# Optimization experiments

Measured on AMD Instinct MI355X. Metric: run time of the kernel, lower is better.

Reference implementation:

```python
import jax, jax.numpy as jnp
import numpy as np
from jax import lax

H = 4096          # hidden_size
NH = 32           # num_attention_heads
NKV = 8           # num_key_value_heads
HD = H // NH      # head_dim = 128
CACHE = 2048      # state_length (kv cache length)
POS = 1024        # current decode position
THETA = 10000.0


def _rope_tables():
    inv_freq = 1.0 / (THETA ** (np.arange(0, HD, 2, dtype=np.float32) / HD))
    t = np.arange(CACHE * 2, dtype=np.float32)
    freqs = np.einsum('i,j->ij', t, inv_freq)          # [2*CACHE, HD/2]
    emb = np.concatenate([freqs, freqs], axis=-1)      # [2*CACHE, HD]
    return (jnp.asarray(np.cos(emb)[None]),            # [1, 2*CACHE, HD]
            jnp.asarray(np.sin(emb)[None]))


def setup_inputs() -> dict:
    key = jax.random.key(0)
    ks = jax.random.split(key, 8)
    cos_cached, sin_cached = _rope_tables()
    # additive causal mask for decode: positions <= current_pos visible
    mask = jnp.where(jnp.arange(CACHE) <= POS, 0.0, -1e9).astype(jnp.float32)
    return {
        'hidden_states': jax.random.normal(ks[0], (1, 1, H), dtype=jnp.float32),
        'attention_mask': mask.reshape(1, 1, 1, CACHE),
        'key_cache': jax.random.normal(ks[1], (1, NKV, CACHE, HD), dtype=jnp.float32),
        'value_cache': jax.random.normal(ks[2], (1, NKV, CACHE, HD), dtype=jnp.float32),
        'q_w': jax.random.normal(ks[3], (NH * HD, H), dtype=jnp.float32) * 0.02,
        'k_w': jax.random.normal(ks[4], (NKV * HD, H), dtype=jnp.float32) * 0.02,
        'v_w': jax.random.normal(ks[5], (NKV * HD, H), dtype=jnp.float32) * 0.02,
        'o_w': jax.random.normal(ks[6], (H, NH * HD), dtype=jnp.float32) * 0.02,
        'cos_cached': cos_cached,
        'sin_cached': sin_cached,
        'position_ids': jnp.full((1, 1), POS, dtype=jnp.int32),
        'current_pos': POS,
    }


def _rotate(x, cos, sin):
    # x: [1, nheads, 1, HD]; cos/sin: [1, 1, 1, HD] (full dim, halves identical)
    half = x.shape[-1] // 2
    x1, x2 = x[..., :half], x[..., half:]
    c, s = cos[..., :half], sin[..., :half]
    return jnp.concatenate([x1 * c - x2 * s, x2 * c + x1 * s], axis=-1)


def reference(hidden_states, attention_mask, key_cache, value_cache,
              q_w, k_w, v_w, o_w, cos_cached, sin_cached,
              position_ids, current_pos):
    # --- QKV projections (1x1 Conv2d == linear) on the single decode token ---
    x = hidden_states[:, 0, :]                           # [1, H]
    q = (x @ q_w.T).reshape(1, NH, 1, HD)
    k = (x @ k_w.T).reshape(1, NKV, 1, HD)
    v = (x @ v_w.T).reshape(1, NKV, 1, HD)

    # --- inline RoPE at current_pos ---
    cos_t = lax.dynamic_slice(cos_cached, (0, current_pos, 0), (1, 1, HD))[:, None]  # [1,1,1,HD]
    sin_t = lax.dynamic_slice(sin_cached, (0, current_pos, 0), (1, 1, HD))[:, None]
    q = _rotate(q, cos_t, sin_t)
    k = _rotate(k, cos_t, sin_t)

    # --- KV-cache append ---
    key_cache = lax.dynamic_update_slice(key_cache, k, (0, 0, current_pos, 0))
    value_cache = lax.dynamic_update_slice(value_cache, v, (0, 0, current_pos, 0))

    # --- GQA scaled dot-product attention over the cache ---
    groups = NH // NKV
    K = jnp.repeat(key_cache, groups, axis=1)            # [1, NH, CACHE, HD]
    V = jnp.repeat(value_cache, groups, axis=1)
    scale = 1.0 / np.sqrt(HD)
    scores = jnp.einsum('bhqd,bhkd->bhqk', q, K) * scale + attention_mask
    attn = jax.nn.softmax(scores, axis=-1)
    ctx = jnp.einsum('bhqk,bhkd->bhqd', attn, V)         # [1, NH, 1, HD]

    # --- output projection ---
    ctx = ctx.transpose(0, 2, 1, 3).reshape(1, 1, NH * HD)
    return jnp.einsum('bsd,od->bso', ctx, o_w)           # [1, 1, H]
```

## Files before the change

### kernel.cpp

```cpp
#include <hip/hip_runtime.h>
#include <math.h>

#define H      4096
#define NH     32
#define NKV    8
#define HD     128
#define CACHE  2048
#define GROUPS (NH / NKV)
#define CHUNK  32
#define NSPL   (CACHE / CHUNK)
#define KSTR   132
#define SCALE  0.08838834764831845f

#define QOFF 0
#define KOFF 4096
#define VOFF 5120
#define POFF 6144
#define PSTRIDE 132
#define CTXOFF (POFF + NH * NSPL * PSTRIDE)

__global__ __launch_bounds__(256) void qkv_gemv(
    const float* __restrict__ x,
    const float* __restrict__ qw, const float* __restrict__ kw,
    const float* __restrict__ vw, float* __restrict__ ws) {
  const int wave = threadIdx.x >> 6;
  const int lane = threadIdx.x & 63;
  const int row  = blockIdx.x * 4 + wave;

  const float* w;
  float* outp;
  int r;
  if (row < 4096)      { w = qw; r = row;        outp = ws + QOFF; }
  else if (row < 5120) { w = kw; r = row - 4096; outp = ws + KOFF; }
  else                 { w = vw; r = row - 5120; outp = ws + VOFF; }

  const float4* wr = (const float4*)(w + (size_t)r * H);
  const float4* xr = (const float4*)x;
  float sum = 0.f;
#pragma unroll
  for (int j = 0; j < H / 4 / 64; ++j) {
    float4 a = wr[j * 64 + lane];
    float4 b = xr[j * 64 + lane];
    sum += a.x * b.x + a.y * b.y + a.z * b.z + a.w * b.w;
  }
#pragma unroll
  for (int off = 32; off > 0; off >>= 1) sum += __shfl_xor(sum, off);
  if (lane == 0) outp[r] = sum;
}

__global__ __launch_bounds__(256) void attn_split(
    const float* __restrict__ kcache, const float* __restrict__ vcache,
    const float* __restrict__ cosc, const float* __restrict__ sinc,
    const int* __restrict__ curp, float* __restrict__ ws) {
  const int kh    = blockIdx.x;
  const int split = blockIdx.y;
  const int cur   = curp[0];
  const int total = cur + 1;
  const int p0    = split * CHUNK;
  if (p0 >= total) return;

  __shared__ float Ks[CHUNK * KSTR];
  __shared__ float Vs[CHUNK * KSTR];
  __shared__ float q_s[GROUPS * HD];
  __shared__ float es[GROUPS][CHUNK];

  const int t = threadIdx.x;

  {
    const int r4 = t >> 5;
    const int c4 = (t & 31) * 4;
    const float* kb = kcache + (size_t)kh * CACHE * HD;
    const float* vb = vcache + (size_t)kh * CACHE * HD;
#pragma unroll
    for (int rr = 0; rr < CHUNK; rr += 8) {
      const int row = rr + r4;
      const int p   = min(p0 + row, cur);
      if (p0 + row != cur) {
        float4 kv = *(const float4*)(kb + (size_t)p * HD + c4);
        float4 vv = *(const float4*)(vb + (size_t)p * HD + c4);
        *(float4*)&Ks[row * KSTR + c4] = kv;
        *(float4*)&Vs[row * KSTR + c4] = vv;
      }
    }
  }
#pragma unroll
  for (int i = 0; i < 2; ++i) {
    const int idx = t + i * 256;
    const int qh = idx >> 7, d = idx & 127;
    const int h = kh * GROUPS + qh;
    const float c  = cosc[(size_t)cur * HD + d];
    const float s  = sinc[(size_t)cur * HD + d];
    const float x1 = ws[QOFF + h * HD + d];
    const float x2 = (d < HD / 2) ? -ws[QOFF + h * HD + d + HD / 2]
                                  :  ws[QOFF + h * HD + d - HD / 2];
    q_s[qh * HD + d] = x1 * c + x2 * s;
  }
  if (cur >= p0 && cur < p0 + CHUNK) {
    const int row = cur - p0;
    if (t < HD) {
      const int d = t;
      const float c  = cosc[(size_t)cur * HD + d];
      const float s  = sinc[(size_t)cur * HD + d];
      const float k1 = ws[KOFF + kh * HD + d];
      const float k2 = (d < HD / 2) ? -ws[KOFF + kh * HD + d + HD / 2]
                                    :  ws[KOFF + kh * HD + d - HD / 2];
      Ks[row * KSTR + d] = k1 * c + k2 * s;
    } else if (t < 2 * HD) {
      const int d = t - HD;
      Vs[row * KSTR + d] = ws[VOFF + kh * HD + d];
    }
  }
  __syncthreads();

  if (t < 128) {
    const int qh = t >> 5, pos = t & 31;
    float4 a = make_float4(0.f, 0.f, 0.f, 0.f);
#pragma unroll
    for (int j = 0; j < HD / 4; ++j) {
      float4 kv = *(const float4*)&Ks[pos * KSTR + j * 4];
      float4 qv = *(const float4*)&q_s[qh * HD + j * 4];
      a.x += kv.x * qv.x; a.y += kv.y * qv.y;
      a.z += kv.z * qv.z; a.w += kv.w * qv.w;
    }
    float s = (a.x + a.y + a.z + a.w) * SCALE;
    const bool valid = (p0 + pos) < total;
    s = valid ? s : -INFINITY;
    float m = s;
#pragma unroll
    for (int off = 16; off > 0; off >>= 1) m = fmaxf(m, __shfl_xor(m, off));
    const float e = valid ? __expf(s - m) : 0.f;
    float l = e;
#pragma unroll
    for (int off = 16; off > 0; off >>= 1) l += __shfl_xor(l, off);
    es[qh][pos] = e;
    if (pos == 0) {
      float* part = ws + POFF + (size_t)((kh * GROUPS + qh) * NSPL + split) * PSTRIDE;
      part[0] = m; part[1] = l;
    }
  }
  __syncthreads();

  {
    const int qh = t >> 6;
    const int d0 = (t & 63) * 2;
    float2 acc = make_float2(0.f, 0.f);
#pragma unroll
    for (int pos = 0; pos < CHUNK; ++pos) {
      const float w = es[qh][pos];
      const float2 vv = *(const float2*)&Vs[pos * KSTR + d0];
      acc.x += w * vv.x; acc.y += w * vv.y;
    }
    float* part = ws + POFF + (size_t)((kh * GROUPS + qh) * NSPL + split) * PSTRIDE;
    part[4 + d0]     = acc.x;
    part[4 + d0 + 1] = acc.y;
  }
}

__global__ __launch_bounds__(128) void attn_combine(
    const int* __restrict__ curp, float* __restrict__ ws) {
  const int h = blockIdx.x;
  const int t = threadIdx.x;
  const int total = curp[0] + 1;
  const int nspl = (total + CHUNK - 1) / CHUNK;
  __shared__ float wsh[64];
  __shared__ float Lsh;

  if (t < 64) {
    float mt = -INFINITY, lt = 0.f;
    if (t < nspl) {
      const float* part = ws + POFF + (size_t)(h * NSPL + t) * PSTRIDE;
      mt = part[0]; lt = part[1];
    }
    float M = mt;
#pragma unroll
    for (int off = 32; off > 0; off >>= 1) M = fmaxf(M, __shfl_xor(M, off));
    const float w = (t < nspl) ? __expf(mt - M) : 0.f;
    float lw = lt * w;
#pragma unroll
    for (int off = 32; off > 0; off >>= 1) lw += __shfl_xor(lw, off);
    wsh[t] = w;
    if (t == 0) Lsh = lw;
  }
  __syncthreads();

  const float Linv = 1.f / Lsh;
  float acc = 0.f;
#pragma unroll 8
  for (int i = 0; i < nspl; ++i)
    acc += wsh[i] * ws[POFF + (size_t)(h * NSPL + i) * PSTRIDE + 4 + t];
  ws[CTXOFF + h * HD + t] = acc * Linv;
}

__global__ __launch_bounds__(256) void o_gemv(
    const float* __restrict__ ow, const float* __restrict__ ws,
    float* __restrict__ out) {
  const int wave = threadIdx.x >> 6;
  const int lane = threadIdx.x & 63;
  const int row  = blockIdx.x * 4 + wave;
  const float4* wr = (const float4*)(ow + (size_t)row * H);
  const float4* xr = (const float4*)(ws + CTXOFF);
  float sum = 0.f;
#pragma unroll
  for (int j = 0; j < H / 4 / 64; ++j) {
    float4 a = wr[j * 64 + lane];
    float4 b = xr[j * 64 + lane];
    sum += a.x * b.x + a.y * b.y + a.z * b.z + a.w * b.w;
  }
#pragma unroll
  for (int off = 32; off > 0; off >>= 1) sum += __shfl_xor(sum, off);
  if (lane == 0) out[row] = sum;
}

extern "C" void kernel_launch(void* const* d_in, const int* in_sizes, int n_in,
                              void* d_out, int out_size, void* d_ws, size_t ws_size,
                              hipStream_t stream) {
  const float* hs   = (const float*)d_in[0];
  const float* kc   = (const float*)d_in[2];
  const float* vc   = (const float*)d_in[3];
  const float* qw   = (const float*)d_in[4];
  const float* kw   = (const float*)d_in[5];
  const float* vw   = (const float*)d_in[6];
  const float* ow   = (const float*)d_in[7];
  const float* cosc = (const float*)d_in[8];
  const float* sinc = (const float*)d_in[9];
  const int*   cur  = (const int*)d_in[11];
  float* ws  = (float*)d_ws;
  float* out = (float*)d_out;

  qkv_gemv<<<1536, 256, 0, stream>>>(hs, qw, kw, vw, ws);
  attn_split<<<dim3(NKV, NSPL), 256, 0, stream>>>(kc, vc, cosc, sinc, cur, ws);
  attn_combine<<<NH, 128, 0, stream>>>(cur, ws);
  o_gemv<<<1024, 256, 0, stream>>>(ow, ws, out);
}
```

Baseline: 42.65 us.

## Fuse split-KV combine into attention via last-block atomic and use one-row-per-block GEMV

```diff
diff --git a/kernel.cpp b/kernel.cpp
--- a/kernel.cpp
+++ b/kernel.cpp
@@ -18,14 +18,16 @@
 #define POFF 6144
 #define PSTRIDE 132
 #define CTXOFF (POFF + NH * NSPL * PSTRIDE)
+#define CNTOFF (CTXOFF + 4096)
 
 __global__ __launch_bounds__(256) void qkv_gemv(
     const float* __restrict__ x,
     const float* __restrict__ qw, const float* __restrict__ kw,
     const float* __restrict__ vw, float* __restrict__ ws) {
-  const int wave = threadIdx.x >> 6;
-  const int lane = threadIdx.x & 63;
-  const int row  = blockIdx.x * 4 + wave;
+  const int t   = threadIdx.x;
+  const int row = blockIdx.x;
+
+  if (row == 0 && t < NKV) ((int*)(ws + CNTOFF))[t] = 0;
 
   const float* w;
   float* outp;
@@ -36,16 +38,21 @@
 
   const float4* wr = (const float4*)(w + (size_t)r * H);
   const float4* xr = (const float4*)x;
+
   float sum = 0.f;
 #pragma unroll
-  for (int j = 0; j < H / 4 / 64; ++j) {
-    float4 a = wr[j * 64 + lane];
-    float4 b = xr[j * 64 + lane];
-    sum += a.x * b.x + a.y * b.y + a.z * b.z + a.w * b.w;
+  for (int i = 0; i < 4; ++i) {
+    const float4 a = wr[i * 256 + t];
+    const float4 b = xr[i * 256 + t];
+    sum = fmaf(a.x, b.x, sum); sum = fmaf(a.y, b.y, sum);
+    sum = fmaf(a.z, b.z, sum); sum = fmaf(a.w, b.w, sum);
   }
 #pragma unroll
   for (int off = 32; off > 0; off >>= 1) sum += __shfl_xor(sum, off);
-  if (lane == 0) outp[r] = sum;
+  __shared__ float red[4];
+  if ((t & 63) == 0) red[t >> 6] = sum;
+  __syncthreads();
+  if (t == 0) outp[r] = red[0] + red[1] + red[2] + red[3];
 }
 
 __global__ __launch_bounds__(256) void attn_split(
@@ -58,11 +65,15 @@
   const int total = cur + 1;
   const int p0    = split * CHUNK;
   if (p0 >= total) return;
+  const int nactive = (total + CHUNK - 1) / CHUNK;
 
   __shared__ float Ks[CHUNK * KSTR];
   __shared__ float Vs[CHUNK * KSTR];
   __shared__ float q_s[GROUPS * HD];
   __shared__ float es[GROUPS][CHUNK];
+  __shared__ float cw[GROUPS][64];
+  __shared__ float cLinv[GROUPS];
+  __shared__ int   lastflag;
 
   const int t = threadIdx.x;
 
@@ -154,61 +165,70 @@
     part[4 + d0]     = acc.x;
     part[4 + d0 + 1] = acc.y;
   }
-}
-
-__global__ __launch_bounds__(128) void attn_combine(
-    const int* __restrict__ curp, float* __restrict__ ws) {
-  const int h = blockIdx.x;
-  const int t = threadIdx.x;
-  const int total = curp[0] + 1;
-  const int nspl = (total + CHUNK - 1) / CHUNK;
-  __shared__ float wsh[64];
-  __shared__ float Lsh;
-
-  if (t < 64) {
+
+  if (t == 0) {
+    __threadfence();
+    int* cnt = (int*)(ws + CNTOFF);
+    const int old = __hip_atomic_fetch_add(&cnt[kh], 1, __ATOMIC_ACQ_REL,
+                                           __HIP_MEMORY_SCOPE_AGENT);
+    lastflag = (old == nactive - 1);
+  }
+  __syncthreads();
+  if (!lastflag) return;
+
+  {
+    const int qh   = t >> 6;
+    const int lane = t & 63;
+    const float* pb = ws + POFF + (size_t)((kh * GROUPS + qh) * NSPL) * PSTRIDE;
     float mt = -INFINITY, lt = 0.f;
-    if (t < nspl) {
-      const float* part = ws + POFF + (size_t)(h * NSPL + t) * PSTRIDE;
-      mt = part[0]; lt = part[1];
-    }
+    if (lane < nactive) { mt = pb[lane * PSTRIDE]; lt = pb[lane * PSTRIDE + 1]; }
     float M = mt;
 #pragma unroll
     for (int off = 32; off > 0; off >>= 1) M = fmaxf(M, __shfl_xor(M, off));
-    const float w = (t < nspl) ? __expf(mt - M) : 0.f;
-    float lw = lt * w;
+    const float wgt = (lane < nactive) ? __expf(mt - M) : 0.f;
+    float lw = lt * wgt;
 #pragma unroll
     for (int off = 32; off > 0; off >>= 1) lw += __shfl_xor(lw, off);
-    wsh[t] = w;
-    if (t == 0) Lsh = lw;
-  }
-  __syncthreads();
-
-  const float Linv = 1.f / Lsh;
-  float acc = 0.f;
-#pragma unroll 8
-  for (int i = 0; i < nspl; ++i)
-    acc += wsh[i] * ws[POFF + (size_t)(h * NSPL + i) * PSTRIDE + 4 + t];
-  ws[CTXOFF + h * HD + t] = acc * Linv;
+    cw[qh][lane] = wgt;
+    if (lane == 0) cLinv[qh] = 1.f / lw;
+  }
+  __syncthreads();
+#pragma unroll
+  for (int i = 0; i < 2; ++i) {
+    const int idx = t + i * 256;
+    const int hh  = idx >> 7;
+    const int d   = idx & 127;
+    const float* pb = ws + POFF + (size_t)((kh * GROUPS + hh) * NSPL) * PSTRIDE;
+    float acc = 0.f;
+    for (int s = 0; s < nactive; ++s)
+      acc += cw[hh][s] * pb[s * PSTRIDE + 4 + d];
+    ws[CTXOFF + (kh * GROUPS + hh) * HD + d] = acc * cLinv[hh];
+  }
 }
 
 __global__ __launch_bounds__(256) void o_gemv(
     const float* __restrict__ ow, const float* __restrict__ ws,
     float* __restrict__ out) {
-  const int wave = threadIdx.x >> 6;
-  const int lane = threadIdx.x & 63;
-  const int row  = blockIdx.x * 4 + wave;
+  const int t   = threadIdx.x;
+  const int row = blockIdx.x;
+
   const float4* wr = (const float4*)(ow + (size_t)row * H);
   const float4* xr = (const float4*)(ws + CTXOFF);
+
   float sum = 0.f;
 #pragma unroll
-  for (int j = 0; j < H / 4 / 64; ++j) {
-    float4 a = wr[j * 64 + lane];
-    float4 b = xr[j * 64 + lane];
-    sum += a.x * b.x + a.y * b.y + a.z * b.z + a.w * b.w;
+  for (int i = 0; i < 4; ++i) {
+    const float4 a = wr[i * 256 + t];
+    const float4 b = xr[i * 256 + t];
+    sum = fmaf(a.x, b.x, sum); sum = fmaf(a.y, b.y, sum);
+    sum = fmaf(a.z, b.z, sum); sum = fmaf(a.w, b.w, sum);
   }
 #pragma unroll
   for (int off = 32; off > 0; off >>= 1) sum += __shfl_xor(sum, off);
-  if (lane == 0) out[row] = sum;
+  __shared__ float red[4];
+  if ((t & 63) == 0) red[t >> 6] = sum;
+  __syncthreads();
+  if (t == 0) out[row] = red[0] + red[1] + red[2] + red[3];
 }
 
 extern "C" void kernel_launch(void* const* d_in, const int* in_sizes, int n_in,
@@ -227,8 +247,7 @@
   float* ws  = (float*)d_ws;
   float* out = (float*)d_out;
 
-  qkv_gemv<<<1536, 256, 0, stream>>>(hs, qw, kw, vw, ws);
+  qkv_gemv<<<6144, 256, 0, stream>>>(hs, qw, kw, vw, ws);
   attn_split<<<dim3(NKV, NSPL), 256, 0, stream>>>(kc, vc, cosc, sinc, cur, ws);
-  attn_combine<<<NH, 128, 0, stream>>>(cur, ws);
-  o_gemv<<<1024, 256, 0, stream>>>(ow, ws, out);
-}
+  o_gemv<<<4096, 256, 0, stream>>>(ow, ws, out);
+}
```

Measured after the change: 50.88 us. 19.3% more time.
